# Kernel tuning notes

Measured on AMD Instinct MI355X. Metric: run time of the kernel, lower is better.

Reference implementation:

```python
import jax, jax.numpy as jnp
import numpy as np

N_EMBD = 1024
N_HEAD = 16
HEAD_DIM = N_EMBD // N_HEAD  # 64
KV_RANK = 256
Q_RANK = 512
ROPE_DIM = 32
B, T = 2, 2048
EPS = 1e-6


def _rope_tables(T, dim):
    inv_freq = 1.0 / (10000.0 ** (np.arange(0, dim, 2, dtype=np.float32) / dim))
    t = np.arange(T, dtype=np.float32)
    freqs = np.outer(t, inv_freq)            # [T, dim/2]
    emb = np.concatenate([freqs, freqs], -1)  # [T, dim]
    return jnp.asarray(np.cos(emb)), jnp.asarray(np.sin(emb))


def _apply_rope(x, cos, sin):
    # x: [B, H, T, D]; cos/sin: [T, D]
    d2 = x.shape[-1] // 2
    x1, x2 = x[..., :d2], x[..., d2:]
    rot = jnp.concatenate([-x2, x1], axis=-1)
    return x * cos[None, None, :, :] + rot * sin[None, None, :, :]


def setup_inputs() -> dict:
    key = jax.random.key(0)
    ks = jax.random.split(key, 10)
    def w(k, fan_in, fan_out):
        return jax.random.normal(k, (fan_in, fan_out), dtype=jnp.float32) * (fan_in ** -0.5)
    return {
        "x": jax.random.normal(ks[0], (B, T, N_EMBD), dtype=jnp.float32),
        "W_kv": w(ks[1], N_EMBD, KV_RANK),
        "g_kv": jnp.ones((KV_RANK,), dtype=jnp.float32),
        "W_kdec": w(ks[2], KV_RANK, N_HEAD * HEAD_DIM),
        "W_vdec": w(ks[3], KV_RANK, N_HEAD * HEAD_DIM),
        "W_q": w(ks[4], N_EMBD, Q_RANK),
        "W_qdec": w(ks[5], Q_RANK, N_HEAD * HEAD_DIM),
        "W_krope": w(ks[6], N_EMBD, N_HEAD * ROPE_DIM),
        "W_qrope": w(ks[7], Q_RANK, N_HEAD * ROPE_DIM),
        "W_o": w(ks[8], N_HEAD * HEAD_DIM, N_EMBD),
    }


def reference(x, W_kv, g_kv, W_kdec, W_vdec, W_q, W_qdec, W_krope, W_qrope, W_o):
    Bx, Tx, C = x.shape
    # low-rank compression
    kv_c = x @ W_kv                                    # [B,T,R_kv]
    kv_c = kv_c * jax.lax.rsqrt(jnp.mean(kv_c * kv_c, axis=-1, keepdims=True) + EPS) * g_kv
    q_c = x @ W_q                                       # [B,T,R_q]
    # decompress to per-head content / rope parts -> [B,H,T,D]
    def heads(y, d):
        return y.reshape(Bx, Tx, N_HEAD, d).transpose(0, 2, 1, 3)
    k_content = heads(kv_c @ W_kdec, HEAD_DIM)
    v = heads(kv_c @ W_vdec, HEAD_DIM)
    q_content = heads(q_c @ W_qdec, HEAD_DIM)
    k_rope = heads(x @ W_krope, ROPE_DIM)
    q_rope = heads(q_c @ W_qrope, ROPE_DIM)
    cos, sin = _rope_tables(Tx, ROPE_DIM)
    q_rope = _apply_rope(q_rope, cos, sin)
    k_rope = _apply_rope(k_rope, cos, sin)
    q = jnp.concatenate([q_content, q_rope], axis=-1)   # [B,H,T,D+Dr]
    k = jnp.concatenate([k_content, k_rope], axis=-1)
    scale = 1.0 / jnp.sqrt(jnp.float32(q.shape[-1]))
    scores = jnp.einsum('bhqd,bhkd->bhqk', q, k) * scale  # [B,H,T,T]
    causal = jnp.tril(jnp.ones((Tx, Tx), dtype=bool))
    scores = jnp.where(causal[None, None], scores, jnp.float32(-jnp.inf))
    attn = jax.nn.softmax(scores, axis=-1)
    out = jnp.einsum('bhqk,bhkd->bhqd', attn, v)          # [B,H,T,D]
    out = out.transpose(0, 2, 1, 3).reshape(Bx, Tx, N_HEAD * HEAD_DIM)
    return out @ W_o
```

## Files before the change

### kernel.cpp

```cpp
#include <hip/hip_runtime.h>
#include <hip/hip_bf16.h>
#include <math.h>

#define Bz 2
#define Tz 2048
#define Cz 1024
#define Hz 16
#define Dz 64
#define Rz 32
#define KVR 256
#define QR 512
#define DQK 96
#define Mz (Bz*Tz)
#define BHT (Bz*Hz*Tz)
#define QK_SCALE 0.10206207261596577f

typedef __attribute__((ext_vector_type(8))) short short8;
typedef __attribute__((ext_vector_type(4))) float f32x4;
typedef __attribute__((ext_vector_type(4))) unsigned short ushort4v;

__device__ __forceinline__ unsigned short f2bf(float f) {
    union { float f; unsigned u; } un; un.f = f;
    unsigned r = un.u + 0x7FFF + ((un.u >> 16) & 1);
    return (unsigned short)(r >> 16);
}

__device__ __forceinline__ void gload_lds16(const void* g, void* l) {
    __builtin_amdgcn_global_load_lds(
        (const __attribute__((address_space(1))) unsigned int*)g,
        (__attribute__((address_space(3))) unsigned int*)l, 16, 0, 0);
}

__global__ __launch_bounds__(256) void conv_f32_bf16(const float* __restrict__ in,
                                                     unsigned short* __restrict__ out,
                                                     int n)
{
    int i = (blockIdx.x * 256 + threadIdx.x) * 4;
    if (i >= n) return;
    float4 v = *(const float4*)&in[i];
    ushort4v o = { f2bf(v.x), f2bf(v.y), f2bf(v.z), f2bf(v.w) };
    *(ushort4v*)&out[i] = o;
}

struct TDesc8 {
    const float* src[8];
    unsigned short* dst[8];
    int K[8], N[8];
    int tile0[9];
};

__global__ __launch_bounds__(256) void transpose_all(TDesc8 p)
{
    __shared__ float ts[32][33];
    int t = blockIdx.x;
    int wi = 0;
    #pragma unroll
    for (int i = 0; i < 7; i++) if (t >= p.tile0[i + 1]) wi = i + 1;
    int lt = t - p.tile0[wi];
    int K = p.K[wi], N = p.N[wi];
    int kT = K >> 5;
    int k0 = (lt % kT) * 32, n0 = (lt / kT) * 32;
    const float* in = p.src[wi];
    unsigned short* out = p.dst[wi];

    int tid = threadIdx.x;
    int r = tid >> 5, cc = tid & 31;
    #pragma unroll
    for (int l = 0; l < 4; l++)
        ts[r + l * 8][cc] = in[(size_t)(k0 + r + l * 8) * N + n0 + cc];
    __syncthreads();
    #pragma unroll
    for (int l = 0; l < 4; l++)
        out[(size_t)(n0 + r + l * 8) * K + k0 + cc] = f2bf(ts[cc][r + l * 8]);
}

template<int EMODE>
__global__ __launch_bounds__(64) void gemm1w(
    const unsigned short* __restrict__ A, const unsigned short* __restrict__ Wt,
    void* __restrict__ O0, void* __restrict__ O1, void* __restrict__ O2,
    int K, float scale)
{
    __shared__ __attribute__((aligned(16))) unsigned short As[64 * 64];
    __shared__ __attribute__((aligned(16))) unsigned short Bs[64 * 64];

    const int lane = threadIdx.x;
    const int c = lane & 15, g = lane >> 4;
    const int m0 = blockIdx.x * 64, n0 = blockIdx.y * 64;
    const int rl = lane >> 3, c8 = lane & 7;

    f32x4 acc[4][4] = {};

    auto stage = [&](int k0) {
        if (EMODE == 4) {
            int h = k0 >> 6;
            #pragma unroll
            for (int i = 0; i < 8; i++) {
                int m = m0 + i * 8 + rl;
                int b = m >> 11, t = m & (Tz - 1);
                gload_lds16(&A[(((size_t)b * Hz + h) * Tz + t) * 64 + c8 * 8],
                            &As[(i * 64 + lane) * 8]);
            }
        } else {
            #pragma unroll
            for (int i = 0; i < 8; i++)
                gload_lds16(&A[(size_t)(m0 + i * 8 + rl) * K + k0 + c8 * 8],
                            &As[(i * 64 + lane) * 8]);
        }
        #pragma unroll
        for (int i = 0; i < 8; i++)
            gload_lds16(&Wt[(size_t)(n0 + i * 8 + rl) * K + k0 + c8 * 8],
                        &Bs[(i * 64 + lane) * 8]);
    };

    stage(0);

    for (int k0 = 0; k0 < K; k0 += 64) {
        asm volatile("s_waitcnt vmcnt(0)" ::: "memory");
        __builtin_amdgcn_sched_barrier(0);

        short8 af[2][4], bfr[2][4];
        #pragma unroll
        for (int ks = 0; ks < 2; ks++) {
            #pragma unroll
            for (int mq = 0; mq < 4; mq++)
                af[ks][mq] = *(const short8*)&As[(mq * 16 + c) * 64 + ks * 32 + g * 8];
            #pragma unroll
            for (int nt = 0; nt < 4; nt++)
                bfr[ks][nt] = *(const short8*)&Bs[(nt * 16 + c) * 64 + ks * 32 + g * 8];
        }
        asm volatile("s_waitcnt lgkmcnt(0)" ::: "memory");
        __builtin_amdgcn_sched_barrier(0);

        if (k0 + 64 < K) stage(k0 + 64);

        __builtin_amdgcn_s_setprio(1);
        #pragma unroll
        for (int ks = 0; ks < 2; ks++)
            #pragma unroll
            for (int mq = 0; mq < 4; mq++)
                #pragma unroll
                for (int nt = 0; nt < 4; nt++)
                    acc[mq][nt] = __builtin_amdgcn_mfma_f32_16x16x32_bf16(
                        af[ks][mq], bfr[ks][nt], acc[mq][nt], 0, 0, 0);
        __builtin_amdgcn_s_setprio(0);
    }

    #pragma unroll
    for (int mq = 0; mq < 4; mq++) {
        #pragma unroll
        for (int r = 0; r < 4; r++) {
            int m = m0 + mq * 16 + g * 4 + r;
            int b = m >> 11, t = m & (Tz - 1);

            if (EMODE == 1) {
                if (n0 < 256) {
                    #pragma unroll
                    for (int nt = 0; nt < 4; nt++)
                        ((float*)O0)[(size_t)m * 256 + n0 + nt * 16 + c] = acc[mq][nt][r];
                } else if (n0 < 768) {
                    #pragma unroll
                    for (int nt = 0; nt < 4; nt++)
                        ((unsigned short*)O1)[(size_t)m * 512 + (n0 - 256) + nt * 16 + c] =
                            f2bf(acc[mq][nt][r]);
                } else {
                    float inv = __expf(-(float)c * 0.5756462732485114f);
                    float ang = (float)t * inv;
                    float cs = cosf(ang), sn = sinf(ang);
                    #pragma unroll
                    for (int np = 0; np < 4; np += 2) {
                        float v0 = acc[mq][np][r];
                        float v1 = acc[mq][np + 1][r];
                        int col0 = (n0 - 768) + np * 16;
                        int h = col0 >> 5;
                        size_t base = (((size_t)b * Hz + h) * Tz + t) * DQK + 64;
                        ((unsigned short*)O2)[base + c]      = f2bf(v0 * cs - v1 * sn);
                        ((unsigned short*)O2)[base + c + 16] = f2bf(v1 * cs + v0 * sn);
                    }
                }
            } else if (EMODE == 2) {
                if (n0 < 1024) {
                    #pragma unroll
                    for (int nt = 0; nt < 4; nt++) {
                        int n = n0 + nt * 16 + c;
                        int h = n >> 6, dd = n & 63;
                        ((unsigned short*)O0)[(((size_t)b * Hz + h) * Tz + t) * DQK + dd] =
                            f2bf(acc[mq][nt][r] * scale);
                    }
                } else {
                    float inv = __expf(-(float)c * 0.5756462732485114f);
                    float ang = (float)t * inv;
                    float cs = cosf(ang), sn = sinf(ang);
                    #pragma unroll
                    for (int np = 0; np < 4; np += 2) {
                        float v0 = acc[mq][np][r] * scale;
                        float v1 = acc[mq][np + 1][r] * scale;
                        int col0 = (n0 - 1024) + np * 16;
                        int h = col0 >> 5;
                        size_t base = (((size_t)b * Hz + h) * Tz + t) * DQK + 64;
                        ((unsigned short*)O0)[base + c]      = f2bf(v0 * cs - v1 * sn);
                        ((unsigned short*)O0)[base + c + 16] = f2bf(v1 * cs + v0 * sn);
                    }
                }
            } else if (EMODE == 3) {
                if (n0 < 1024) {
                    #pragma unroll
                    for (int nt = 0; nt < 4; nt++) {
                        int n = n0 + nt * 16 + c;
                        int h = n >> 6, dd = n & 63;
                        ((unsigned short*)O0)[(((size_t)b * Hz + h) * Tz + t) * DQK + dd] =
                            f2bf(acc[mq][nt][r]);
                    }
                } else {
                    #pragma unroll
                    for (int nt = 0; nt < 4; nt++) {
                        int n = (n0 - 1024) + nt * 16 + c;
                        int h = n >> 6, dd = n & 63;
                        ((unsigned short*)O1)[(((size_t)b * Hz + h) * 64 + dd) * Tz + t] =
                            f2bf(acc[mq][nt][r]);
                    }
                }
            } else {
                #pragma unroll
                for (int nt = 0; nt < 4; nt++)
                    ((float*)O0)[(size_t)m * 1024 + n0 + nt * 16 + c] = acc[mq][nt][r];
            }
        }
    }
}

__global__ __launch_bounds__(256) void rmsnorm_k(const float* __restrict__ kv,
                                                 const float* __restrict__ g,
                                                 unsigned short* __restrict__ outb)
{
    int row = blockIdx.x * 4 + (threadIdx.x >> 6);
    int lane = threadIdx.x & 63;
    const float* p = kv + (size_t)row * 256;
    float v[4];
    float ss = 0.f;
    #pragma unroll
    for (int i = 0; i < 4; i++) { v[i] = p[lane + i * 64]; ss += v[i] * v[i]; }
    #pragma unroll
    for (int o = 32; o > 0; o >>= 1) ss += __shfl_xor(ss, o);
    float r = rsqrtf(ss * (1.f / 256.f) + 1e-6f);
    #pragma unroll
    for (int i = 0; i < 4; i++)
        outb[(size_t)row * 256 + lane + i * 64] = f2bf(v[i] * r * g[lane + i * 64]);
}

#define KSTR 104
#define PSTR 72

__global__ __launch_bounds__(256, 3) void attn_mfma(
    const unsigned short* __restrict__ q,
    const unsigned short* __restrict__ k,
    const unsigned short* __restrict__ vt,
    unsigned short* __restrict__ o)
{
    __shared__ __attribute__((aligned(16))) unsigned short Ks[2][64 * KSTR];
    __shared__ __attribute__((aligned(16))) unsigned short Ps[4][16 * PSTR];

    int tid = threadIdx.x;
    int lane = tid & 63;
    int w = tid >> 6;
    int c = lane & 15, g = lane >> 4;

    int idx = blockIdx.x;
    int bh = ((idx & 7) << 2) | ((idx >> 3) & 3);
    int qt = 31 - (idx >> 5);
    int q0 = qt * 64;
    int ntiles = qt + 1;

    const unsigned short* qb = q + (size_t)bh * Tz * DQK;
    const unsigned short* kb = k + (size_t)bh * Tz * DQK;
    const unsigned short* vb = vt + (size_t)bh * 64 * Tz;
    unsigned short* ps = &Ps[w][0];

    int srow[3], sc8[3];
    #pragma unroll
    for (int i = 0; i < 3; i++) {
        int id2 = tid + i * 256;
        srow[i] = id2 / 12; sc8[i] = id2 % 12;
    }

    short8 qf[3];
    {
        const unsigned short* qrow = qb + (size_t)(q0 + w * 16 + c) * DQK;
        #pragma unroll
        for (int kc = 0; kc < 3; kc++)
            qf[kc] = *(const short8*)(qrow + kc * 32 + g * 8);
    }

    short8 kreg[3];
    #pragma unroll
    for (int i = 0; i < 3; i++)
        kreg[i] = *(const short8*)&kb[(size_t)srow[i] * DQK + sc8[i] * 8];
    #pragma unroll
    for (int i = 0; i < 3; i++)
        *(short8*)&Ks[0][srow[i] * KSTR + sc8[i] * 8] = kreg[i];
    __syncthreads();

    f32x4 oacc[4] = {};
    float mrun[4], lrun[4];
    #pragma unroll
    for (int r = 0; r < 4; r++) { mrun[r] = -1e30f; lrun[r] = 0.f; }

    for (int t = 0; t < ntiles; t++) {
        int cur = t & 1;
        int kt0 = t * 64;
        bool more = (t + 1) < ntiles;

        if (more) {
            #pragma unroll
            for (int i = 0; i < 3; i++)
                kreg[i] = *(const short8*)&kb[(size_t)(kt0 + 64 + srow[i]) * DQK + sc8[i] * 8];
        }
        short8 vf[2][4];
        #pragma unroll
        for (int kc2 = 0; kc2 < 2; kc2++)
            #pragma unroll
            for (int nt = 0; nt < 4; nt++)
                vf[kc2][nt] = *(const short8*)&vb[(size_t)(nt * 16 + c) * Tz + kt0 + kc2 * 32 + g * 8];

        f32x4 sacc[4] = {};
        __builtin_amdgcn_s_setprio(1);
        #pragma unroll
        for (int kc = 0; kc < 3; kc++) {
            #pragma unroll
            for (int nt = 0; nt < 4; nt++) {
                short8 bfrag = *(const short8*)&Ks[cur][(nt * 16 + c) * KSTR + kc * 32 + g * 8];
                sacc[nt] = __builtin_amdgcn_mfma_f32_16x16x32_bf16(qf[kc], bfrag, sacc[nt], 0, 0, 0);
            }
        }
        __builtin_amdgcn_s_setprio(0);

        if (kt0 == q0) {
            #pragma unroll
            for (int nt = 0; nt < 4; nt++)
                #pragma unroll
                for (int r = 0; r < 4; r++)
                    if (nt * 16 + c > w * 16 + g * 4 + r)
                        sacc[nt][r] = -1e30f;
        }

        float pm[4], rs[4];
        #pragma unroll
        for (int r = 0; r < 4; r++)
            pm[r] = fmaxf(fmaxf(sacc[0][r], sacc[1][r]), fmaxf(sacc[2][r], sacc[3][r]));
        #pragma unroll
        for (int r = 0; r < 4; r++) {
            #pragma unroll
            for (int off = 1; off < 16; off <<= 1)
                pm[r] = fmaxf(pm[r], __shfl_xor(pm[r], off));
        }
        bool need = false;
        #pragma unroll
        for (int r = 0; r < 4; r++) need = need || (pm[r] > mrun[r] + 8.f);

        if (__ballot(need)) {
            float sc[4];
            #pragma unroll
            for (int r = 0; r < 4; r++) {
                float mn = fmaxf(mrun[r], pm[r]);
                sc[r] = __expf(mrun[r] - mn);
                mrun[r] = mn;
            }
            #pragma unroll
            for (int nt = 0; nt < 4; nt++)
                #pragma unroll
                for (int r = 0; r < 4; r++)
                    sacc[nt][r] = __expf(sacc[nt][r] - mrun[r]);
            #pragma unroll
            for (int r = 0; r < 4; r++)
                rs[r] = sacc[0][r] + sacc[1][r] + sacc[2][r] + sacc[3][r];
            #pragma unroll
            for (int r = 0; r < 4; r++) {
                #pragma unroll
                for (int off = 1; off < 16; off <<= 1)
                    rs[r] += __shfl_xor(rs[r], off);
                lrun[r] = lrun[r] * sc[r] + rs[r];
            }
            #pragma unroll
            for (int nt = 0; nt < 4; nt++)
                #pragma unroll
                for (int r = 0; r < 4; r++)
                    oacc[nt][r] *= sc[r];
        } else {
            #pragma unroll
            for (int nt = 0; nt < 4; nt++)
                #pragma unroll
                for (int r = 0; r < 4; r++)
                    sacc[nt][r] = __expf(sacc[nt][r] - mrun[r]);
            #pragma unroll
            for (int r = 0; r < 4; r++)
                rs[r] = sacc[0][r] + sacc[1][r] + sacc[2][r] + sacc[3][r];
            #pragma unroll
            for (int r = 0; r < 4; r++) {
                #pragma unroll
                for (int off = 1; off < 16; off <<= 1)
                    rs[r] += __shfl_xor(rs[r], off);
                lrun[r] += rs[r];
            }
        }

        #pragma unroll
        for (int nt = 0; nt < 4; nt++)
            #pragma unroll
            for (int r = 0; r < 4; r++)
                ps[(g * 4 + r) * PSTR + nt * 16 + c] = f2bf(sacc[nt][r]);
        __builtin_amdgcn_wave_barrier();

        __builtin_amdgcn_s_setprio(1);
        #pragma unroll
        for (int kc2 = 0; kc2 < 2; kc2++) {
            short8 pf = *(const short8*)&ps[c * PSTR + kc2 * 32 + g * 8];
            #pragma unroll
            for (int nt = 0; nt < 4; nt++)
                oacc[nt] = __builtin_amdgcn_mfma_f32_16x16x32_bf16(pf, vf[kc2][nt], oacc[nt], 0, 0, 0);
        }
        __builtin_amdgcn_s_setprio(0);
        __builtin_amdgcn_wave_barrier();

        if (more) {
            #pragma unroll
            for (int i = 0; i < 3; i++)
                *(short8*)&Ks[1 - cur][srow[i] * KSTR + sc8[i] * 8] = kreg[i];
            __syncthreads();
        }
    }

    #pragma unroll
    for (int nt = 0; nt < 4; nt++)
        #pragma unroll
        for (int r = 0; r < 4; r++)
            o[((size_t)bh * Tz + q0 + w * 16 + g * 4 + r) * 64 + nt * 16 + c] =
                f2bf(oacc[nt][r] / lrun[r]);
}

extern "C" void kernel_launch(void* const* d_in, const int* in_sizes, int n_in,
                              void* d_out, int out_size, void* d_ws, size_t ws_size,
                              hipStream_t stream)
{
    const float* x       = (const float*)d_in[0];
    const float* W_kv    = (const float*)d_in[1];
    const float* g_kv    = (const float*)d_in[2];
    const float* W_kdec  = (const float*)d_in[3];
    const float* W_vdec  = (const float*)d_in[4];
    const float* W_q     = (const float*)d_in[5];
    const float* W_qdec  = (const float*)d_in[6];
    const float* W_krope = (const float*)d_in[7];
    const float* W_qrope = (const float*)d_in[8];
    const float* W_o     = (const float*)d_in[9];
    float* out = (float*)d_out;

    float* kv_f32 = (float*)d_ws;
    unsigned short* us = (unsigned short*)(kv_f32 + (size_t)Mz * KVR);
    unsigned short* x_bf  = us;               us += (size_t)Mz * Cz;
    unsigned short* kv_bf = us;               us += (size_t)Mz * KVR;
    unsigned short* qc_bf = us;               us += (size_t)Mz * QR;
    unsigned short* qbb   = us;               us += (size_t)BHT * DQK;
    unsigned short* kbb   = us;               us += (size_t)BHT * DQK;
    unsigned short* vtb   = us;               us += (size_t)BHT * 64;
    unsigned short* ob    = us;               us += (size_t)BHT * 64;
    unsigned short* wc1 = us;                 us += (size_t)1280 * Cz;
    unsigned short* wc2 = us;                 us += (size_t)1536 * QR;
    unsigned short* wc3 = us;                 us += (size_t)2048 * KVR;
    unsigned short* woT = us;                 us += (size_t)Cz * Cz;

    dim3 blk(256);

    conv_f32_bf16<<<dim3((Mz*Cz)/1024), blk, 0, stream>>>(x, x_bf, Mz*Cz);

    TDesc8 td;
    const float* tsrc[8] = {W_kv, W_q, W_krope, W_qdec, W_qrope, W_kdec, W_vdec, W_o};
    unsigned short* tdst[8] = {
        wc1, wc1 + (size_t)256 * Cz, wc1 + (size_t)768 * Cz,
        wc2, wc2 + (size_t)1024 * QR,
        wc3, wc3 + (size_t)1024 * KVR,
        woT };
    int tK[8] = {Cz, Cz, Cz, QR, QR, KVR, KVR, Cz};
    int tN[8] = {KVR, QR, Hz*Rz, Hz*Dz, Hz*Rz, Hz*Dz, Hz*Dz, Cz};
    int cum = 0;
    td.tile0[0] = 0;
    for (int i = 0; i < 8; i++) {
        td.src[i] = tsrc[i]; td.dst[i] = tdst[i]; td.K[i] = tK[i]; td.N[i] = tN[i];
        cum += (tK[i] / 32) * (tN[i] / 32);
        td.tile0[i + 1] = cum;
    }
    transpose_all<<<dim3(cum), blk, 0, stream>>>(td);

    gemm1w<1><<<dim3(Mz/64, 1280/64), dim3(64), 0, stream>>>(
        x_bf, wc1, kv_f32, qc_bf, kbb, Cz, 1.f);
    rmsnorm_k<<<dim3(Mz/4), blk, 0, stream>>>(kv_f32, g_kv, kv_bf);
    gemm1w<2><<<dim3(Mz/64, 1536/64), dim3(64), 0, stream>>>(
        qc_bf, wc2, qbb, nullptr, nullptr, QR, QK_SCALE);
    gemm1w<3><<<dim3(Mz/64, 2048/64), dim3(64), 0, stream>>>(
        kv_bf, wc3, kbb, vtb, nullptr, KVR, 1.f);
    attn_mfma<<<dim3(1024), blk, 0, stream>>>(qbb, kbb, vtb, ob);
    gemm1w<4><<<dim3(Mz/64, Cz/64), dim3(64), 0, stream>>>(
        ob, woT, out, nullptr, nullptr, Cz, 1.f);
}
```

Baseline: 170.2 us.

## Transpose score MFMA so each lane owns one query row, use exp2 softmax

The QK^T MFMA now takes K as the A operand, so each lane holds scores for a single query row. The row max and row sum then need only two cross-lane shuffles instead of four-deep butterflies over four rows. The softmax scale is folded with log2(e) into Q so exp2f can replace __expf, and the rescale threshold is adjusted to match. The K tile in LDS switches from padding to an XOR swizzle, P is packed with v_cvt_pk_bf16_f32, occupancy is raised to 4 blocks, and block ordering changes to interleave long and short causal tiles. The risks are more register pressure at the higher occupancy target and extra shuffles to broadcast the scale factors back to rows.

Result: slower. 247.5 us (+45.4%).

```diff
diff --git a/kernel.cpp b/kernel.cpp
--- a/kernel.cpp
+++ b/kernel.cpp
@@ -14,6 +14,8 @@
 #define Mz (Bz*Tz)
 #define BHT (Bz*Hz*Tz)
 #define QK_SCALE 0.10206207261596577f
+#define QK_SCALE2 0.14724538519399733f
+#define THR2 11.541560327111707f
 
 typedef __attribute__((ext_vector_type(8))) short short8;
 typedef __attribute__((ext_vector_type(4))) float f32x4;
@@ -247,16 +249,15 @@
         outb[(size_t)row * 256 + lane + i * 64] = f2bf(v[i] * r * g[lane + i * 64]);
 }
 
-#define KSTR 104
 #define PSTR 72
 
-__global__ __launch_bounds__(256, 3) void attn_mfma(
+__global__ __launch_bounds__(256, 4) void attn_mfma(
     const unsigned short* __restrict__ q,
     const unsigned short* __restrict__ k,
     const unsigned short* __restrict__ vt,
     unsigned short* __restrict__ o)
 {
-    __shared__ __attribute__((aligned(16))) unsigned short Ks[2][64 * KSTR];
+    __shared__ __attribute__((aligned(16))) unsigned short Ks[2][64 * 96];
     __shared__ __attribute__((aligned(16))) unsigned short Ps[4][16 * PSTR];
 
     int tid = threadIdx.x;
@@ -264,9 +265,10 @@
     int w = tid >> 6;
     int c = lane & 15, g = lane >> 4;
 
-    int idx = blockIdx.x;
-    int bh = ((idx & 7) << 2) | ((idx >> 3) & 3);
-    int qt = 31 - (idx >> 5);
+    int s = blockIdx.x;
+    int bh = s & 31;
+    int j = s >> 5;
+    int qt = (j < 16) ? (31 - j) : (j - 16);
     int q0 = qt * 64;
     int ntiles = qt + 1;
 
@@ -275,11 +277,13 @@
     const unsigned short* vb = vt + (size_t)bh * 64 * Tz;
     unsigned short* ps = &Ps[w][0];
 
-    int srow[3], sc8[3];
+    int soff[3], sidx[3];
     #pragma unroll
     for (int i = 0; i < 3; i++) {
         int id2 = tid + i * 256;
-        srow[i] = id2 / 12; sc8[i] = id2 % 12;
+        int srow = id2 / 12, sc8 = id2 % 12;
+        soff[i] = srow * DQK + sc8 * 8;
+        sidx[i] = (srow * 96 + sc8 * 8) ^ ((srow & 7) << 3);
     }
 
     short8 qf[3];
@@ -293,16 +297,14 @@
     short8 kreg[3];
     #pragma unroll
     for (int i = 0; i < 3; i++)
-        kreg[i] = *(const short8*)&kb[(size_t)srow[i] * DQK + sc8[i] * 8];
+        kreg[i] = *(const short8*)&kb[soff[i]];
     #pragma unroll
     for (int i = 0; i < 3; i++)
-        *(short8*)&Ks[0][srow[i] * KSTR + sc8[i] * 8] = kreg[i];
+        *(short8*)&Ks[0][sidx[i]] = kreg[i];
     __syncthreads();
 
     f32x4 oacc[4] = {};
-    float mrun[4], lrun[4];
-    #pragma unroll
-    for (int r = 0; r < 4; r++) { mrun[r] = -1e30f; lrun[r] = 0.f; }
+    float mrun = -1e30f, lrun = 0.f;
 
     for (int t = 0; t < ntiles; t++) {
         int cur = t & 1;
@@ -312,7 +314,7 @@
         if (more) {
             #pragma unroll
             for (int i = 0; i < 3; i++)
-                kreg[i] = *(const short8*)&kb[(size_t)(kt0 + 64 + srow[i]) * DQK + sc8[i] * 8];
+                kreg[i] = *(const short8*)&kb[(size_t)(kt0 + 64) * DQK + soff[i]];
         }
         short8 vf[2][4];
         #pragma unroll
@@ -327,8 +329,8 @@
         for (int kc = 0; kc < 3; kc++) {
             #pragma unroll
             for (int nt = 0; nt < 4; nt++) {
-                short8 bfrag = *(const short8*)&Ks[cur][(nt * 16 + c) * KSTR + kc * 32 + g * 8];
-                sacc[nt] = __builtin_amdgcn_mfma_f32_16x16x32_bf16(qf[kc], bfrag, sacc[nt], 0, 0, 0);
+                short8 kf = *(const short8*)&Ks[cur][((nt * 16 + c) * 96 + kc * 32 + g * 8) ^ ((c & 7) << 3)];
+                sacc[nt] = __builtin_amdgcn_mfma_f32_16x16x32_bf16(kf, qf[kc], sacc[nt], 0, 0, 0);
             }
         }
         __builtin_amdgcn_s_setprio(0);
@@ -338,75 +340,66 @@
             for (int nt = 0; nt < 4; nt++)
                 #pragma unroll
                 for (int r = 0; r < 4; r++)
-                    if (nt * 16 + c > w * 16 + g * 4 + r)
+                    if (nt * 16 + g * 4 + r > w * 16 + c)
                         sacc[nt][r] = -1e30f;
         }
 
-        float pm[4], rs[4];
-        #pragma unroll
-        for (int r = 0; r < 4; r++)
-            pm[r] = fmaxf(fmaxf(sacc[0][r], sacc[1][r]), fmaxf(sacc[2][r], sacc[3][r]));
-        #pragma unroll
-        for (int r = 0; r < 4; r++) {
-            #pragma unroll
-            for (int off = 1; off < 16; off <<= 1)
-                pm[r] = fmaxf(pm[r], __shfl_xor(pm[r], off));
-        }
-        bool need = false;
-        #pragma unroll
-        for (int r = 0; r < 4; r++) need = need || (pm[r] > mrun[r] + 8.f);
-
+        float pm = sacc[0][0];
+        #pragma unroll
+        for (int nt = 0; nt < 4; nt++)
+            #pragma unroll
+            for (int r = 0; r < 4; r++)
+                pm = fmaxf(pm, sacc[nt][r]);
+        pm = fmaxf(pm, __shfl_xor(pm, 16));
+        pm = fmaxf(pm, __shfl_xor(pm, 32));
+
+        bool need = pm > mrun + THR2;
         if (__ballot(need)) {
-            float sc[4];
-            #pragma unroll
-            for (int r = 0; r < 4; r++) {
-                float mn = fmaxf(mrun[r], pm[r]);
-                sc[r] = __expf(mrun[r] - mn);
-                mrun[r] = mn;
+            float mn = fmaxf(mrun, pm);
+            float sc = exp2f(mrun - mn);
+            mrun = mn;
+            float rs = 0.f;
+            #pragma unroll
+            for (int nt = 0; nt < 4; nt++)
+                #pragma unroll
+                for (int r = 0; r < 4; r++) {
+                    sacc[nt][r] = exp2f(sacc[nt][r] - mrun);
+                    rs += sacc[nt][r];
+                }
+            rs += __shfl_xor(rs, 16);
+            rs += __shfl_xor(rs, 32);
+            lrun = lrun * sc + rs;
+            float scr[4];
+            #pragma unroll
+            for (int r = 0; r < 4; r++) scr[r] = __shfl(sc, g * 4 + r);
+            #pragma unroll
+            for (int nt = 0; nt < 4; nt++)
+                #pragma unroll
+                for (int r = 0; r < 4; r++)
+                    oacc[nt][r] *= scr[r];
+        } else {
+            float rs = 0.f;
+            #pragma unroll
+            for (int nt = 0; nt < 4; nt++)
+                #pragma unroll
+                for (int r = 0; r < 4; r++) {
+                    sacc[nt][r] = exp2f(sacc[nt][r] - mrun);
+                    rs += sacc[nt][r];
+                }
+            rs += __shfl_xor(rs, 16);
+            rs += __shfl_xor(rs, 32);
+            lrun += rs;
+        }
+
+        #pragma unroll
+        for (int nt = 0; nt < 4; nt++)
+            #pragma unroll
+            for (int rp = 0; rp < 2; rp++) {
+                unsigned w32;
+                asm("v_cvt_pk_bf16_f32 %0, %1, %2"
+                    : "=v"(w32) : "v"(sacc[nt][2 * rp]), "v"(sacc[nt][2 * rp + 1]));
+                *(unsigned*)&ps[c * PSTR + nt * 16 + g * 4 + 2 * rp] = w32;
             }
-            #pragma unroll
-            for (int nt = 0; nt < 4; nt++)
-                #pragma unroll
-                for (int r = 0; r < 4; r++)
-                    sacc[nt][r] = __expf(sacc[nt][r] - mrun[r]);
-            #pragma unroll
-            for (int r = 0; r < 4; r++)
-                rs[r] = sacc[0][r] + sacc[1][r] + sacc[2][r] + sacc[3][r];
-            #pragma unroll
-            for (int r = 0; r < 4; r++) {
-                #pragma unroll
-                for (int off = 1; off < 16; off <<= 1)
-                    rs[r] += __shfl_xor(rs[r], off);
-                lrun[r] = lrun[r] * sc[r] + rs[r];
-            }
-            #pragma unroll
-            for (int nt = 0; nt < 4; nt++)
-                #pragma unroll
-                for (int r = 0; r < 4; r++)
-                    oacc[nt][r] *= sc[r];
-        } else {
-            #pragma unroll
-            for (int nt = 0; nt < 4; nt++)
-                #pragma unroll
-                for (int r = 0; r < 4; r++)
-                    sacc[nt][r] = __expf(sacc[nt][r] - mrun[r]);
-            #pragma unroll
-            for (int r = 0; r < 4; r++)
-                rs[r] = sacc[0][r] + sacc[1][r] + sacc[2][r] + sacc[3][r];
-            #pragma unroll
-            for (int r = 0; r < 4; r++) {
-                #pragma unroll
-                for (int off = 1; off < 16; off <<= 1)
-                    rs[r] += __shfl_xor(rs[r], off);
-                lrun[r] += rs[r];
-            }
-        }
-
-        #pragma unroll
-        for (int nt = 0; nt < 4; nt++)
-            #pragma unroll
-            for (int r = 0; r < 4; r++)
-                ps[(g * 4 + r) * PSTR + nt * 16 + c] = f2bf(sacc[nt][r]);
         __builtin_amdgcn_wave_barrier();
 
         __builtin_amdgcn_s_setprio(1);
@@ -423,17 +416,20 @@
         if (more) {
             #pragma unroll
             for (int i = 0; i < 3; i++)
-                *(short8*)&Ks[1 - cur][srow[i] * KSTR + sc8[i] * 8] = kreg[i];
+                *(short8*)&Ks[1 - cur][sidx[i]] = kreg[i];
             __syncthreads();
         }
     }
 
+    float lr[4];
+    #pragma unroll
+    for (int r = 0; r < 4; r++) lr[r] = __shfl(lrun, g * 4 + r);
     #pragma unroll
     for (int nt = 0; nt < 4; nt++)
         #pragma unroll
         for (int r = 0; r < 4; r++)
             o[((size_t)bh * Tz + q0 + w * 16 + g * 4 + r) * 64 + nt * 16 + c] =
-                f2bf(oacc[nt][r] / lrun[r]);
+                f2bf(oacc[nt][r] / lr[r]);
 }
 
 extern "C" void kernel_launch(void* const* d_in, const int* in_sizes, int n_in,
@@ -492,7 +488,7 @@
         x_bf, wc1, kv_f32, qc_bf, kbb, Cz, 1.f);
     rmsnorm_k<<<dim3(Mz/4), blk, 0, stream>>>(kv_f32, g_kv, kv_bf);
     gemm1w<2><<<dim3(Mz/64, 1536/64), dim3(64), 0, stream>>>(
-        qc_bf, wc2, qbb, nullptr, nullptr, QR, QK_SCALE);
+        qc_bf, wc2, qbb, nullptr, nullptr, QR, QK_SCALE2);
     gemm1w<3><<<dim3(Mz/64, 2048/64), dim3(64), 0, stream>>>(
         kv_bf, wc3, kbb, vtb, nullptr, KVR, 1.f);
     attn_mfma<<<dim3(1024), blk, 0, stream>>>(qbb, kbb, vtb, ob);
```
